# Kernel tuning notes

Measured on AMD Instinct MI355X. Metric: run time of the kernel, lower is better.

The kernel has to match this reference:

```python
import jax, jax.numpy as jnp
import numpy as np

D_MODEL = 1024
D_K = 64
D_V = 64
H = 16
B = 4
S = 2048
NEG = -1000000000.0


def setup_inputs() -> dict:
    key = jax.random.key(0)
    ks = jax.random.split(key, 6)
    x = jax.random.normal(ks[0], (B, S, D_MODEL), dtype=jnp.float32)
    # mask: 1 = pad, 0 = valid (per module's `mask = 1 - mask` convention)
    mask = jax.random.randint(ks[1], (B, S), 0, 2, dtype=jnp.int32)
    sc = 1.0 / np.sqrt(D_MODEL)
    Wq = jax.random.normal(ks[2], (D_K * H, D_MODEL), dtype=jnp.float32) * sc
    Wk = jax.random.normal(ks[3], (D_K * H, D_MODEL), dtype=jnp.float32) * sc
    Wv = jax.random.normal(ks[4], (D_V * H, D_MODEL), dtype=jnp.float32) * sc
    Wo = jax.random.normal(ks[5], (D_MODEL, D_V * H), dtype=jnp.float32) * (1.0 / np.sqrt(D_V * H))
    return {"x": x, "mask": mask, "Wq": Wq, "Wk": Wk, "Wv": Wv, "Wo": Wo}


def _split_heads(y, h):
    b, s, _ = y.shape
    return y.reshape(b, s, h, -1).transpose(0, 2, 1, 3)  # [B,H,S,d]


def reference(x, mask, Wq, Wk, Wv, Wo):
    # valid = 1 - mask (1 where token is valid); bidirectional pad mask = outer product
    valid = (1 - mask).astype(x.dtype)  # [B,S]
    pair = valid[:, None, :, None] * valid[:, None, None, :]  # [B,1,S,S]
    q = _split_heads(x @ Wq.T, H)  # [B,H,S,dk]
    k = _split_heads(x @ Wk.T, H)
    v = _split_heads(x @ Wv.T, H)
    qk = jnp.einsum("bhqd,bhkd->bhqk", q, k) / jnp.sqrt(jnp.asarray(D_K, x.dtype))
    qk = jnp.where(pair == 0, jnp.asarray(NEG, x.dtype), qk)
    attn = jax.nn.softmax(qk, axis=-1)  # dropout omitted (eval mode)
    heads = jnp.einsum("bhqk,bhkd->bhqd", attn, v)
    concat = heads.transpose(0, 2, 1, 3).reshape(x.shape[0], x.shape[1], -1)
    return concat @ Wo.T
```

## Files before the change

kernel.cpp:

```cpp
#include <hip/hip_runtime.h>
#include <stdint.h>


typedef __bf16 bf16;
typedef __bf16 bf16x8 __attribute__((ext_vector_type(8)));
typedef __bf16 bf16x4 __attribute__((ext_vector_type(4)));
typedef float f32x4 __attribute__((ext_vector_type(4)));
typedef float f32x16 __attribute__((ext_vector_type(16)));

#define DM    1024
#define NH    16
#define SS    2048
#define BB    4
#define NTOK  8192
#define QKVLD 3072
#define LOG2E_DIV8 0.18033688011112042f
#define CSHIFT 12.0f

__device__ __forceinline__ int swz(int row, int byteoff) {
    return byteoff ^ ((row & 7) << 4);
}
__device__ __forceinline__ float fexp2(float x) {
    float r; asm("v_exp_f32 %0, %1" : "=v"(r) : "v"(x)); return r;
}
__device__ __forceinline__ uint32_t cvtpk(float lo, float hi_) {
    uint32_t r; asm("v_cvt_pk_bf16_f32 %0, %1, %2" : "=v"(r) : "v"(lo), "v"(hi_)); return r;
}
__device__ __forceinline__ void gload_lds16(const void* g, void* l) {
    __builtin_amdgcn_global_load_lds(
        (const __attribute__((address_space(1))) uint32_t*)g,
        (__attribute__((address_space(3))) uint32_t*)l, 16, 0, 0);
}

__global__ void cvt_kernel(const float* __restrict__ in, bf16* __restrict__ out, int n8) {
    int i = blockIdx.x * blockDim.x + threadIdx.x;
    if (i >= n8) return;
    const float4* p = reinterpret_cast<const float4*>(in) + (size_t)i * 2;
    float4 a = p[0], b = p[1];
    bf16x8 o;
    o[0] = (bf16)a.x; o[1] = (bf16)a.y; o[2] = (bf16)a.z; o[3] = (bf16)a.w;
    o[4] = (bf16)b.x; o[5] = (bf16)b.y; o[6] = (bf16)b.z; o[7] = (bf16)b.w;
    reinterpret_cast<bf16x8*>(out)[i] = o;
}

__global__ void wcvt_kernel(const float* __restrict__ wq, const float* __restrict__ wk,
                            const float* __restrict__ wv, const float* __restrict__ wo,
                            bf16* __restrict__ wqkv, bf16* __restrict__ wob) {
    int i = blockIdx.x * blockDim.x + threadIdx.x;
    int seg = i >> 17, off = i & 131071;
    const float* src = (seg == 0) ? wq : (seg == 1) ? wk : (seg == 2) ? wv : wo;
    bf16* dst = (seg < 3) ? (wqkv + (size_t)seg * DM * DM) : wob;
    const float4* p = reinterpret_cast<const float4*>(src) + (size_t)off * 2;
    float4 a = p[0], b = p[1];
    bf16x8 o;
    o[0] = (bf16)a.x; o[1] = (bf16)a.y; o[2] = (bf16)a.z; o[3] = (bf16)a.w;
    o[4] = (bf16)b.x; o[5] = (bf16)b.y; o[6] = (bf16)b.z; o[7] = (bf16)b.w;
    reinterpret_cast<bf16x8*>(dst)[off] = o;
}

__global__ void biasprep_kernel(const int* __restrict__ mask, float* __restrict__ bias) {
    int idx = blockIdx.x * blockDim.x + threadIdx.x;
    if (idx >= 4 * 2048) return;
    int e = idx & 15, hi = (idx >> 4) & 1, kg = (idx >> 5) & 3;
    int kt = (idx >> 7) & 15, b = idx >> 11;
    int key = kt * 128 + kg * 32 + 4 * hi + 8 * (e >> 2) + (e & 3);
    bias[idx] = mask[b * SS + key] ? -__builtin_inff() : -CSHIFT;
}

template <typename OT>
__global__ __launch_bounds__(256) void gemm_bt(
    const bf16* __restrict__ A, int lda, const bf16* __restrict__ Bm, OT* __restrict__ C,
    int M, int N, int K)
{
    __shared__ bf16 As[128 * 64];
    __shared__ bf16 Bs[128 * 64];

    const int nwg = gridDim.x * gridDim.y;
    const int wg = blockIdx.y * gridDim.x + blockIdx.x;
    const int nsw = (wg & 7) * (nwg >> 3) + (wg >> 3);
    const int tn = nsw % gridDim.x, tm = nsw / gridDim.x;

    const int tid = threadIdx.x;
    const int lane = tid & 63, wv = tid >> 6;
    const int wr = wv >> 1, wc = wv & 1;
    const int lr = lane & 15, lg = lane >> 4;

    const f32x4 zero = {0.f, 0.f, 0.f, 0.f};
    f32x4 acc[4][4];
#pragma unroll
    for (int mi = 0; mi < 4; ++mi)
#pragma unroll
        for (int ni = 0; ni < 4; ++ni) acc[mi][ni] = zero;

    const char* Abase = (const char*)(A + (size_t)(tm * 128) * lda);
    const char* Bbase = (const char*)(Bm + (size_t)(tn * 128) * K);

    for (int k0 = 0; k0 < K; k0 += 64) {
#pragma unroll
        for (int i = 0; i < 4; ++i) {
            int idx = tid + 256 * i;
            int row = idx >> 3, ch = idx & 7;
            int gcol = (ch * 16) ^ ((row & 7) << 4);
            gload_lds16(Abase + (size_t)row * (lda * 2) + k0 * 2 + gcol, (char*)As + idx * 16);
            gload_lds16(Bbase + (size_t)row * (K * 2) + k0 * 2 + gcol, (char*)Bs + idx * 16);
        }
        __syncthreads();

#pragma unroll
        for (int ks = 0; ks < 2; ++ks) {
            bf16x8 af[4], bfr[4];
#pragma unroll
            for (int mi = 0; mi < 4; ++mi) {
                int row = wr * 64 + mi * 16 + lr;
                af[mi] = *reinterpret_cast<const bf16x8*>(
                    (char*)As + swz(row, row * 128 + ks * 64 + lg * 16));
            }
#pragma unroll
            for (int ni = 0; ni < 4; ++ni) {
                int row = wc * 64 + ni * 16 + lr;
                bfr[ni] = *reinterpret_cast<const bf16x8*>(
                    (char*)Bs + swz(row, row * 128 + ks * 64 + lg * 16));
            }
#pragma unroll
            for (int mi = 0; mi < 4; ++mi)
#pragma unroll
                for (int ni = 0; ni < 4; ++ni)
                    acc[mi][ni] = __builtin_amdgcn_mfma_f32_16x16x32_bf16(
                        af[mi], bfr[ni], acc[mi][ni], 0, 0, 0);
        }
        __syncthreads();
    }

#pragma unroll
    for (int mi = 0; mi < 4; ++mi)
#pragma unroll
        for (int ni = 0; ni < 4; ++ni)
#pragma unroll
            for (int r = 0; r < 4; ++r) {
                int row = tm * 128 + wr * 64 + mi * 16 + lg * 4 + r;
                int col = tn * 128 + wc * 64 + ni * 16 + lr;
                C[(size_t)row * N + col] = (OT)acc[mi][ni][r];
            }
}

__global__ __launch_bounds__(256) void vtrans_kernel(
    const bf16* __restrict__ vb, int ldv, bf16* __restrict__ vT)
{
    const int st = blockIdx.x, bh = blockIdx.y;
    const int b = bh >> 4, h = bh & 15;
    const int tid = threadIdx.x;
    __shared__ bf16 T[64 * 64];
#pragma unroll
    for (int i = 0; i < 2; ++i) {
        int idx = tid + 256 * i;
        int s = idx >> 3, ch = idx & 7;
        bf16x8 v = *reinterpret_cast<const bf16x8*>(
            vb + (size_t)(b * SS + st * 64 + s) * ldv + h * 64 + ch * 8);
        *reinterpret_cast<bf16x8*>((char*)T + swz(s, s * 128 + ch * 16)) = v;
    }
    __syncthreads();
#pragma unroll
    for (int i = 0; i < 2; ++i) {
        int idx = tid + 256 * i;
        int d = idx >> 3, ch = idx & 7;
        bf16x8 o;
#pragma unroll
        for (int j = 0; j < 8; ++j) {
            int s = ch * 8 + j;
            o[j] = *reinterpret_cast<const bf16*>((char*)T + swz(s, s * 128 + d * 2));
        }
        *reinterpret_cast<bf16x8*>(vT + ((size_t)bh * 64 + d) * SS + st * 64 + ch * 8) = o;
    }
}

__global__ __launch_bounds__(512) void attn_kernel(
    const bf16* __restrict__ qkv, const bf16* __restrict__ vT,
    const float* __restrict__ bias, const int* __restrict__ mask,
    bf16* __restrict__ concat)
{
    const int w = blockIdx.x;
    const int nw = (w & 7) * 64 + (w >> 3);
    const int qt = nw & 7, bh = nw >> 3;
    const int b = bh >> 4, h = bh & 15;
    const int tid = threadIdx.x;
    const int lane = tid & 63, wv = tid >> 6;
    const int lq = lane & 31, hi = lane >> 5;

    __shared__ bf16 Ks[2][128 * 64];
    __shared__ bf16 Vs[2][64 * 128];
    __shared__ float Bl[2048 + 16];

    const size_t tok0 = (size_t)b * SS;
    const int qrow0 = qt * 256 + wv * 32;

    const int qpad = mask[tok0 + qrow0 + lq];
    bf16x8 qf[4];
    {
        const bf16* qp = qkv + (tok0 + qrow0 + lq) * QKVLD + h * 64 + hi * 8;
#pragma unroll
        for (int ks = 0; ks < 4; ++ks) {
            bf16x8 v = *reinterpret_cast<const bf16x8*>(qp + ks * 16);
#pragma unroll
            for (int j = 0; j < 8; ++j)
                v[j] = qpad ? (bf16)0.f : (bf16)((float)v[j] * LOG2E_DIV8);
            qf[ks] = v;
        }
    }
    bf16x8 ones;
#pragma unroll
    for (int j = 0; j < 8; ++j) ones[j] = (bf16)1.0f;

    f32x16 oA, oB, lacc;
#pragma unroll
    for (int e = 0; e < 16; ++e) { oA[e] = 0.f; oB[e] = 0.f; lacc[e] = 0.f; }

    const int c0 = tid, c1 = tid + 512;
    const int kr0 = c0 >> 3, kc0 = c0 & 7, kr1 = c1 >> 3, kc1 = c1 & 7;
    const int vr0 = c0 >> 4, vc0 = c0 & 15, vr1 = c1 >> 4, vc1 = c1 & 15;
    const char* kSrc = (const char*)(qkv + 1024 + h * 64);
    const char* vSrc = (const char*)(vT + (size_t)bh * 64 * SS);
    const size_t kOff0 = (tok0 + kr0) * (QKVLD * 2) + ((kc0 * 16) ^ ((kr0 & 7) << 4));
    const size_t kOff1 = (tok0 + kr1) * (QKVLD * 2) + ((kc1 * 16) ^ ((kr1 & 7) << 4));
    const size_t vOff0 = (size_t)vr0 * (SS * 2) + ((vc0 * 16) ^ ((vr0 & 15) << 4));
    const size_t vOff1 = (size_t)vr1 * (SS * 2) + ((vc1 * 16) ^ ((vr1 & 15) << 4));

    const int kxor = (hi * 16) ^ ((lq & 7) << 4);
    const int vxor = (hi * 16) ^ ((lq & 15) << 4);
    const int bmask = qpad ? 0 : -1;
    const char* bbase = (const char*)Bl + (qpad ? 8192 : hi * 64);

    gload_lds16(kSrc + kOff0, (char*)Ks[0] + c0 * 16);
    gload_lds16(kSrc + kOff1, (char*)Ks[0] + c1 * 16);
    gload_lds16(vSrc + vOff0, (char*)Vs[0] + c0 * 16);
    gload_lds16(vSrc + vOff1, (char*)Vs[0] + c1 * 16);
    gload_lds16((const char*)(bias + (size_t)b * 2048) + tid * 16, (char*)Bl + tid * 16);
    if (tid < 4) {
        f32x4 z = {-CSHIFT, -CSHIFT, -CSHIFT, -CSHIFT};
        *reinterpret_cast<f32x4*>((char*)Bl + 8192 + tid * 16) = z;
    }
    __syncthreads();

    for (int kt = 0; kt < 16; ++kt) {
        const int cur = kt & 1;

        if (kt < 15) {
            const size_t kAdv = (size_t)(kt + 1) * 128 * (QKVLD * 2);
            const size_t vAdv = (size_t)(kt + 1) * 256;
            gload_lds16(kSrc + kOff0 + kAdv, (char*)Ks[cur ^ 1] + c0 * 16);
            gload_lds16(kSrc + kOff1 + kAdv, (char*)Ks[cur ^ 1] + c1 * 16);
            gload_lds16(vSrc + vOff0 + vAdv, (char*)Vs[cur ^ 1] + c0 * 16);
            gload_lds16(vSrc + vOff1 + vAdv, (char*)Vs[cur ^ 1] + c1 * 16);
        }

        const char* kB = (const char*)Ks[cur];
        const char* vB = (const char*)Vs[cur];
        const int bo = (kt * 512) & bmask;

        f32x16 s[4];
#pragma unroll
        for (int kg = 0; kg < 4; ++kg)
            s[kg] = *reinterpret_cast<const f32x16*>(bbase + bo + ((kg * 128) & bmask));
        __builtin_amdgcn_s_setprio(1);
#pragma unroll
        for (int kg = 0; kg < 4; ++kg) {
            const char* kR = kB + (kg * 32 + lq) * 128;
#pragma unroll
            for (int ks = 0; ks < 4; ++ks) {
                bf16x8 kf = *reinterpret_cast<const bf16x8*>(kR + (kxor ^ (ks * 32)));
                s[kg] = __builtin_amdgcn_mfma_f32_32x32x16_bf16(kf, qf[ks], s[kg], 0, 0, 0);
            }
        }
        __builtin_amdgcn_s_setprio(0);

#pragma unroll
        for (int kg = 0; kg < 4; ++kg)
#pragma unroll
            for (int e = 0; e < 16; ++e)
                s[kg][e] = fexp2(s[kg][e]);

        __builtin_amdgcn_s_setprio(1);
#pragma unroll
        for (int kk = 0; kk < 8; ++kk) {
            const float* pp = (const float*)&s[kk >> 1];
            const int ks2 = kk & 1;
            uint32_t c0p = cvtpk(pp[8 * ks2 + 0], pp[8 * ks2 + 1]);
            uint32_t c1p = cvtpk(pp[8 * ks2 + 2], pp[8 * ks2 + 3]);
            uint32_t c2p = cvtpk(pp[8 * ks2 + 4], pp[8 * ks2 + 5]);
            uint32_t c3p = cvtpk(pp[8 * ks2 + 6], pp[8 * ks2 + 7]);
            asm("v_permlane32_swap_b32 %0, %1" : "+v"(c0p), "+v"(c2p));
            asm("v_permlane32_swap_b32 %0, %1" : "+v"(c1p), "+v"(c3p));
            union { uint32_t u[4]; bf16x8 v; } pu;
            pu.u[0] = c0p; pu.u[1] = c1p; pu.u[2] = c2p; pu.u[3] = c3p;
            bf16x8 vf0 = *reinterpret_cast<const bf16x8*>(
                vB + (lq)*256 + (vxor ^ (kk * 32)));
            bf16x8 vf1 = *reinterpret_cast<const bf16x8*>(
                vB + (32 + lq) * 256 + (vxor ^ (kk * 32)));
            oA = __builtin_amdgcn_mfma_f32_32x32x16_bf16(vf0, pu.v, oA, 0, 0, 0);
            oB = __builtin_amdgcn_mfma_f32_32x32x16_bf16(vf1, pu.v, oB, 0, 0, 0);
            lacc = __builtin_amdgcn_mfma_f32_32x32x16_bf16(ones, pu.v, lacc, 0, 0, 0);
        }
        __builtin_amdgcn_s_setprio(0);

        if (kt < 15) __syncthreads();
    }

    float inv = 1.0f / lacc[0];
#pragma unroll
    for (int g = 0; g < 4; ++g) {
        bf16x4 w0, w1;
#pragma unroll
        for (int r = 0; r < 4; ++r) {
            w0[r] = (bf16)(oA[g * 4 + r] * inv);
            w1[r] = (bf16)(oB[g * 4 + r] * inv);
        }
        int d0 = 4 * hi + 8 * g;
        bf16* cp = concat + (tok0 + qrow0 + lq) * QKVLD + h * 64 + d0;
        *reinterpret_cast<bf16x4*>(cp) = w0;
        *reinterpret_cast<bf16x4*>(cp + 32) = w1;
    }
}

extern "C" void kernel_launch(void* const* d_in, const int* in_sizes, int n_in,
                              void* d_out, int out_size, void* d_ws, size_t ws_size,
                              hipStream_t stream)
{
    const float* x  = (const float*)d_in[0];
    const int* mask = (const int*)d_in[1];
    const float* Wq = (const float*)d_in[2];
    const float* Wk = (const float*)d_in[3];
    const float* Wv = (const float*)d_in[4];
    const float* Wo = (const float*)d_in[5];
    float* out = (float*)d_out;

    char* ws = (char*)d_ws;
    bf16* xb    = (bf16*)(ws);
    bf16* wqkv  = (bf16*)(ws + (16ull << 20));
    bf16* wob   = (bf16*)(ws + (22ull << 20));
    bf16* qkv   = (bf16*)(ws + (24ull << 20));
    bf16* vT    = xb;
    float* bias = (float*)wqkv;
    bf16* concat = qkv + 2048;

    cvt_kernel<<<dim3((NTOK * DM / 8) / 256), 256, 0, stream>>>(x, xb, NTOK * DM / 8);
    wcvt_kernel<<<dim3(2048), 256, 0, stream>>>(Wq, Wk, Wv, Wo, wqkv, wob);

    gemm_bt<bf16><<<dim3(QKVLD / 128, NTOK / 128), 256, 0, stream>>>(
        xb, DM, wqkv, qkv, NTOK, QKVLD, DM);

    vtrans_kernel<<<dim3(SS / 64, BB * NH), 256, 0, stream>>>(qkv + 2048, QKVLD, vT);
    biasprep_kernel<<<dim3(32), 256, 0, stream>>>(mask, bias);

    attn_kernel<<<dim3((SS / 256) * (BB * NH)), 512, 0, stream>>>(
        qkv, vT, bias, mask, concat);

    gemm_bt<float><<<dim3(DM / 128, NTOK / 128), 256, 0, stream>>>(
        concat, QKVLD, wob, out, NTOK, DM, DM);
}
```

Measured before the change: 192.5 us.

## Add 256x256-tile double-buffered GEMM kernel for the QKV projection

Adds a new bf16 GEMM kernel with 256x256 output tiles, 512 threads (8 waves, each computing 128x64) and a two-stage LDS double buffer fed by direct global-to-LDS loads, with MFMA priority hints. The QKV projection now uses this kernel instead of the 128x128 one. The aim is more data reuse per LDS byte and load/compute overlap. In exchange it uses 128KB of LDS per block, so only one block fits per CU. The grid shrinks to 384 blocks, which can leave a partially idle second wave across the CUs.

Result: slower. 209.6 us (+8.9%).

```diff
diff --git a/kernel.cpp b/kernel.cpp
--- a/kernel.cpp
+++ b/kernel.cpp
@@ -65,6 +65,114 @@
     int kt = (idx >> 7) & 15, b = idx >> 11;
     int key = kt * 128 + kg * 32 + 4 * hi + 8 * (e >> 2) + (e & 3);
     bias[idx] = mask[b * SS + key] ? -__builtin_inff() : -CSHIFT;
+}
+
+__global__ __launch_bounds__(512, 2) void gemm_bt256(
+    const bf16* __restrict__ A, int lda, const bf16* __restrict__ Bm,
+    bf16* __restrict__ C, int M, int N, int K)
+{
+    __shared__ bf16 As[2][2][128 * 64];
+    __shared__ bf16 Bs[2][2][128 * 64];
+
+    const int nwg = gridDim.x * gridDim.y;
+    const int wg = blockIdx.y * gridDim.x + blockIdx.x;
+    const int nsw = (wg & 7) * (nwg >> 3) + (wg >> 3);
+    const int tn = nsw % gridDim.x, tm = nsw / gridDim.x;
+
+    const int tid = threadIdx.x;
+    const int lane = tid & 63, wv = tid >> 6;
+    const int wm = wv >> 2, wn = wv & 3;
+    const int lr = lane & 15, lg = lane >> 4;
+
+    f32x4 acc[8][4];
+#pragma unroll
+    for (int mi = 0; mi < 8; ++mi)
+#pragma unroll
+        for (int ni = 0; ni < 4; ++ni) {
+            f32x4 z = {0.f, 0.f, 0.f, 0.f};
+            acc[mi][ni] = z;
+        }
+
+    const int r0 = tid >> 3, c0 = tid & 7;
+    const int r1 = (tid + 512) >> 3, c1 = tid & 7;
+    const int g0 = (c0 * 16) ^ ((r0 & 7) << 4);
+    const int g1 = (c1 * 16) ^ ((r1 & 7) << 4);
+    const char* Ab = (const char*)(A + (size_t)(tm * 256) * lda);
+    const char* Bb = (const char*)(Bm + (size_t)(tn * 256) * K);
+    const size_t ldaB = (size_t)lda * 2, ldbB = (size_t)K * 2;
+
+    auto stage = [&](int t) {
+        const int buf = t & 1;
+        const size_t kb = (size_t)t * 128;
+#pragma unroll
+        for (int h = 0; h < 2; ++h) {
+            gload_lds16(Ab + (size_t)(h * 128 + r0) * ldaB + kb + g0, (char*)As[buf][h] + tid * 16);
+            gload_lds16(Ab + (size_t)(h * 128 + r1) * ldaB + kb + g1, (char*)As[buf][h] + (tid + 512) * 16);
+            gload_lds16(Bb + (size_t)(h * 128 + r0) * ldbB + kb + g0, (char*)Bs[buf][h] + tid * 16);
+            gload_lds16(Bb + (size_t)(h * 128 + r1) * ldbB + kb + g1, (char*)Bs[buf][h] + (tid + 512) * 16);
+        }
+    };
+
+    const int nkt = K >> 6;
+    stage(0);
+    stage(1);
+
+    for (int t = 0; t < nkt; ++t) {
+        const int buf = t & 1;
+        if (t + 1 < nkt) asm volatile("s_waitcnt vmcnt(8)" ::: "memory");
+        else             asm volatile("s_waitcnt vmcnt(0)" ::: "memory");
+        __builtin_amdgcn_s_barrier();
+
+        const char* Ah = (const char*)As[buf][wm];
+        const char* Bh = (const char*)Bs[buf][wn >> 1];
+        const int bbase = (wn & 1) * 64;
+
+#pragma unroll
+        for (int mh = 0; mh < 2; ++mh) {
+            bf16x8 af[4][2];
+#pragma unroll
+            for (int mi = 0; mi < 4; ++mi) {
+                int row = (mh * 4 + mi) * 16 + lr;
+#pragma unroll
+                for (int ks = 0; ks < 2; ++ks)
+                    af[mi][ks] = *reinterpret_cast<const bf16x8*>(
+                        Ah + swz(row, row * 128 + ks * 64 + lg * 16));
+            }
+#pragma unroll
+            for (int nh = 0; nh < 2; ++nh) {
+                __builtin_amdgcn_s_setprio(1);
+#pragma unroll
+                for (int ni = 0; ni < 2; ++ni) {
+                    int row = bbase + (nh * 2 + ni) * 16 + lr;
+                    bf16x8 b0 = *reinterpret_cast<const bf16x8*>(
+                        Bh + swz(row, row * 128 + lg * 16));
+                    bf16x8 b1 = *reinterpret_cast<const bf16x8*>(
+                        Bh + swz(row, row * 128 + 64 + lg * 16));
+#pragma unroll
+                    for (int mi = 0; mi < 4; ++mi) {
+                        acc[mh * 4 + mi][nh * 2 + ni] = __builtin_amdgcn_mfma_f32_16x16x32_bf16(
+                            af[mi][0], b0, acc[mh * 4 + mi][nh * 2 + ni], 0, 0, 0);
+                        acc[mh * 4 + mi][nh * 2 + ni] = __builtin_amdgcn_mfma_f32_16x16x32_bf16(
+                            af[mi][1], b1, acc[mh * 4 + mi][nh * 2 + ni], 0, 0, 0);
+                    }
+                }
+                __builtin_amdgcn_s_setprio(0);
+            }
+        }
+        __builtin_amdgcn_s_barrier();
+        if (t + 2 < nkt) stage(t + 2);
+    }
+
+#pragma unroll
+    for (int mi = 0; mi < 8; ++mi)
+#pragma unroll
+        for (int ni = 0; ni < 4; ++ni)
+#pragma unroll
+            for (int r = 0; r < 4; ++r) {
+                int row = tm * 256 + wm * 128 + mi * 16 + lg * 4 + r;
+                int col = tn * 256 + wn * 64 + ni * 16 + lr;
+                C[(size_t)row * N + col] = (bf16)acc[mi][ni][r];
+            }
 }
 
 template <typename OT>
@@ -344,7 +452,7 @@
     cvt_kernel<<<dim3((NTOK * DM / 8) / 256), 256, 0, stream>>>(x, xb, NTOK * DM / 8);
     wcvt_kernel<<<dim3(2048), 256, 0, stream>>>(Wq, Wk, Wv, Wo, wqkv, wob);
 
-    gemm_bt<bf16><<<dim3(QKVLD / 128, NTOK / 128), 256, 0, stream>>>(
+    gemm_bt256<<<dim3(QKVLD / 256, NTOK / 256), 512, 0, stream>>>(
         xb, DM, wqkv, qkv, NTOK, QKVLD, DM);
 
     vtrans_kernel<<<dim3(SS / 64, BB * NH), 256, 0, stream>>>(qkv + 2048, QKVLD, vT);
```
